# Kernel tuning notes

Measured on AMD Instinct MI355X. Metric: run time of the kernel, lower is better.

The kernel has to match this reference:

```python
import jax, jax.numpy as jnp
import numpy as np

N, E = 50000, 800000
IN_DIM, HID, HEADS, LAYERS = 128, 128, 4, 2
C = HID // HEADS  # per-head channels
LN_EPS = 1e-5


def _segment_softmax(logits, seg, num_segments):
    # logits: [E, H], seg: [E] target-node ids
    m = jax.ops.segment_max(logits, seg, num_segments=num_segments)  # [N, H]
    ex = jnp.exp(logits - m[seg])
    s = jax.ops.segment_sum(ex, seg, num_segments=num_segments)      # [N, H]
    return ex / s[seg]


def setup_inputs() -> dict:
    key = jax.random.key(0)
    ks = jax.random.split(key, 16)
    x = jax.random.normal(ks[0], (N, IN_DIM), dtype=jnp.float32)
    edge_index = jax.random.randint(ks[1], (2, E), 0, N, dtype=jnp.int64)
    edge_weight = jax.random.normal(ks[2], (E,), dtype=jnp.float32)
    s = 0.05
    # stacked per-layer params (in_ch == hidden for both layers since in_dim == hidden_dim)
    Wq = jax.random.normal(ks[3], (LAYERS, HID, HID), dtype=jnp.float32) * s
    bq = jnp.zeros((LAYERS, HID), dtype=jnp.float32)
    Wk = jax.random.normal(ks[4], (LAYERS, HID, HID), dtype=jnp.float32) * s
    bk = jnp.zeros((LAYERS, HID), dtype=jnp.float32)
    Wv = jax.random.normal(ks[5], (LAYERS, HID, HID), dtype=jnp.float32) * s
    bv = jnp.zeros((LAYERS, HID), dtype=jnp.float32)
    We = jax.random.normal(ks[6], (LAYERS, 1, HID), dtype=jnp.float32) * s  # lin_edge, no bias
    Wskip = jax.random.normal(ks[7], (LAYERS, HID, HID), dtype=jnp.float32) * s
    bskip = jnp.zeros((LAYERS, HID), dtype=jnp.float32)
    ln_g = jnp.ones((LAYERS, HID), dtype=jnp.float32)
    ln_b = jnp.zeros((LAYERS, HID), dtype=jnp.float32)
    return dict(x=x, edge_index=edge_index, edge_weight=edge_weight,
                Wq=Wq, bq=bq, Wk=Wk, bk=bk, Wv=Wv, bv=bv, We=We,
                Wskip=Wskip, bskip=bskip, ln_g=ln_g, ln_b=ln_b)


def reference(x, edge_index, edge_weight, Wq, bq, Wk, bk, Wv, bv, We, Wskip, bskip, ln_g, ln_b):
    # eval mode: dropout (on alpha and on features) is identity
    h = jnp.nan_to_num(x, nan=0.0, posinf=0.0, neginf=0.0)
    edge_attr = jnp.nan_to_num(edge_weight, nan=0.0, posinf=0.0, neginf=0.0)[:, None]  # [E,1]
    src, dst = edge_index[0], edge_index[1]  # PyG: x_j = x[src], softmax/aggregate over dst
    scale = 1.0 / jnp.sqrt(jnp.asarray(C, dtype=h.dtype))
    for l in range(LAYERS):
        h_res = h
        q = (h @ Wq[l] + bq[l]).reshape(N, HEADS, C)
        k = (h @ Wk[l] + bk[l]).reshape(N, HEADS, C)
        v = (h @ Wv[l] + bv[l]).reshape(N, HEADS, C)
        e = (edge_attr @ We[l]).reshape(E, HEADS, C)          # lin_edge (bias=False)
        kj = k[src] + e                                       # [E,H,C]
        logits = jnp.einsum('ehc,ehc->eh', q[dst], kj) * scale
        alpha = _segment_softmax(logits, dst, N)              # [E,H]
        msg = (v[src] + e) * alpha[..., None]                 # [E,H,C]
        out = jax.ops.segment_sum(msg, dst, num_segments=N).reshape(N, HID)
        out = out + h @ Wskip[l] + bskip[l]                   # root_weight skip (beta=False)
        out = jnp.nan_to_num(out, nan=0.0, posinf=0.0, neginf=0.0)
        mu = out.mean(axis=-1, keepdims=True)
        var = ((out - mu) ** 2).mean(axis=-1, keepdims=True)
        out = (out - mu) / jnp.sqrt(var + LN_EPS) * ln_g[l] + ln_b[l]
        out = jax.nn.relu(jnp.nan_to_num(out, nan=0.0, posinf=0.0, neginf=0.0))
        out = jnp.nan_to_num(out, nan=0.0, posinf=0.0, neginf=0.0)
        h = jnp.nan_to_num(out + h_res, nan=0.0, posinf=0.0, neginf=0.0)
    return h
```

## Files before the change

kernel.cpp:

```cpp
#include <hip/hip_runtime.h>
#include <hip/hip_fp16.h>
#include <math.h>

#define NN 50000
#define EE 800000
#define HID 128
#define LAYERS 2
#define LN_EPS 1e-5f
#define SCALE 0.17677669529663687f
#define NB 49

typedef _Float16 f16x8 __attribute__((ext_vector_type(8)));
typedef _Float16 h2 __attribute__((ext_vector_type(2)));
typedef float f32x4 __attribute__((ext_vector_type(4)));

__device__ __forceinline__ float sanitize(float f) {
    return (f == f && fabsf(f) != INFINITY) ? f : 0.0f;
}


__global__ void zero_deg_kernel(int* __restrict__ deg) {
    int i = blockIdx.x * blockDim.x + threadIdx.x;
    if (i < NN) deg[i] = 0;
}

__global__ void hist_kernel(const int* __restrict__ eidx, int* __restrict__ deg) {
    int e = blockIdx.x * blockDim.x + threadIdx.x;
    if (e < EE) atomicAdd(&deg[eidx[EE + e]], 1);
}


__global__ __launch_bounds__(1024) void deg_bsum_kernel(const int* __restrict__ deg,
                                                        int* __restrict__ bsum) {
    __shared__ int red[16];
    int tid = threadIdx.x;
    int i = blockIdx.x * 1024 + tid;
    int v = (i < NN) ? deg[i] : 0;
    #pragma unroll
    for (int off = 32; off >= 1; off >>= 1) v += __shfl_xor(v, off, 64);
    if ((tid & 63) == 0) red[tid >> 6] = v;
    __syncthreads();
    if (tid == 0) {
        int s = 0;
        #pragma unroll
        for (int w = 0; w < 16; ++w) s += red[w];
        bsum[blockIdx.x] = s;
    }
}

__global__ void bsum_scan_kernel(const int* __restrict__ bsum, int* __restrict__ boff,
                                 int* __restrict__ row_start) {
    int lane = threadIdx.x;
    int v = (lane < NB) ? bsum[lane] : 0;
    int sc = v;
    #pragma unroll
    for (int off = 1; off < 64; off <<= 1) {
        int t = __shfl_up(sc, off, 64);
        if (lane >= off) sc += t;
    }
    if (lane < NB) boff[lane] = sc - v;
    if (lane == 63) row_start[NN] = sc;
}

__global__ __launch_bounds__(1024) void deg_scan_kernel(const int* __restrict__ deg,
                                                        const int* __restrict__ boff,
                                                        int* __restrict__ row_start,
                                                        int* __restrict__ cursor) {
    __shared__ int wsum[16];
    int tid = threadIdx.x;
    int lane = tid & 63;
    int wid = tid >> 6;
    int i = blockIdx.x * 1024 + tid;
    int val = (i < NN) ? deg[i] : 0;
    int sc = val;
    #pragma unroll
    for (int off = 1; off < 64; off <<= 1) {
        int t = __shfl_up(sc, off, 64);
        if (lane >= off) sc += t;
    }
    if (lane == 63) wsum[wid] = sc;
    __syncthreads();
    if (wid == 0) {
        int s = (lane < 16) ? wsum[lane] : 0;
        #pragma unroll
        for (int off = 1; off < 16; off <<= 1) {
            int t = __shfl_up(s, off, 64);
            if (lane >= off) s += t;
        }
        if (lane < 16) wsum[lane] = s;
    }
    __syncthreads();
    int waveoff = (wid > 0) ? wsum[wid - 1] : 0;
    int excl = boff[blockIdx.x] + waveoff + sc - val;
    if (i < NN) {
        row_start[i] = excl;
        cursor[i] = excl;
    }
}

__global__ void scatter_kernel(const int* __restrict__ eidx,
                               const float* __restrict__ ew,
                               int* __restrict__ cursor,
                               long long* __restrict__ csr_pk) {
    int e = blockIdx.x * blockDim.x + threadIdx.x;
    if (e < EE) {
        int dst = eidx[EE + e];
        int src = eidx[e];
        int pos = atomicAdd(&cursor[dst], 1);
        unsigned wb = __float_as_uint(sanitize(ew[e]));
        csr_pk[pos] = ((long long)wb << 32) | (unsigned)src;
    }
}


__global__ void sanitize_kernel(const float* __restrict__ x, float* __restrict__ h0,
                                __half* __restrict__ hh) {
    int i = blockIdx.x * blockDim.x + threadIdx.x;
    if (i < NN * HID / 4) {
        float4 f = ((const float4*)x)[i];
        f.x = sanitize(f.x); f.y = sanitize(f.y); f.z = sanitize(f.z); f.w = sanitize(f.w);
        ((float4*)h0)[i] = f;
        __half2* hp = (__half2*)(hh + (size_t)i * 4);
        hp[0] = __floats2half2_rn(f.x, f.y);
        hp[1] = __floats2half2_rn(f.z, f.w);
    }
}


__global__ void wtcvt_kernel(const float* __restrict__ Wq, const float* __restrict__ Wk,
                             const float* __restrict__ Wv, const float* __restrict__ Wsk,
                             __half* __restrict__ WT) {
    int idx = blockIdx.x * blockDim.x + threadIdx.x;
    if (idx >= LAYERS * 4 * HID * HID) return;
    int k = idx & 127;
    int c = (idx >> 7) & 127;
    int m = (idx >> 14) & 3;
    int l = idx >> 16;
    const float* W = (m == 0) ? Wq : (m == 1) ? Wk : (m == 2) ? Wv : Wsk;
    WT[idx] = __float2half(W[l * HID * HID + k * HID + c]);
}


__global__ __launch_bounds__(256) void mfma_qkvs_kernel(
    const __half* __restrict__ hh, const __half* __restrict__ WT,
    const float* __restrict__ bq, const float* __restrict__ bk,
    const float* __restrict__ bv, const float* __restrict__ bsk,
    __half* __restrict__ qh, __half* __restrict__ kv, float* __restrict__ skf)
{
    int wid = threadIdx.x >> 6;
    int lane = threadIdx.x & 63;
    int row0 = blockIdx.x * 64 + wid * 16;
    int arow = row0 + (lane & 15);
    if (arow >= NN) arow = NN - 1;
    int ksub = (lane >> 4) * 8;

    const _Float16* hp = (const _Float16*)(hh + (size_t)arow * HID + ksub);
    f16x8 a0 = *(const f16x8*)(hp + 0);
    f16x8 a1 = *(const f16x8*)(hp + 32);
    f16x8 a2 = *(const f16x8*)(hp + 64);
    f16x8 a3 = *(const f16x8*)(hp + 96);

    #pragma unroll
    for (int m = 0; m < 4; ++m) {
        const _Float16* Wm = (const _Float16*)(WT + m * HID * HID);
        const float* bias = (m == 0) ? bq : (m == 1) ? bk : (m == 2) ? bv : bsk;
        #pragma unroll
        for (int t = 0; t < 8; ++t) {
            int col = t * 16 + (lane & 15);
            const _Float16* wc = Wm + (size_t)col * HID + ksub;
            f32x4 acc = {0.f, 0.f, 0.f, 0.f};
            acc = __builtin_amdgcn_mfma_f32_16x16x32_f16(a0, *(const f16x8*)(wc + 0),  acc, 0, 0, 0);
            acc = __builtin_amdgcn_mfma_f32_16x16x32_f16(a1, *(const f16x8*)(wc + 32), acc, 0, 0, 0);
            acc = __builtin_amdgcn_mfma_f32_16x16x32_f16(a2, *(const f16x8*)(wc + 64), acc, 0, 0, 0);
            acc = __builtin_amdgcn_mfma_f32_16x16x32_f16(a3, *(const f16x8*)(wc + 96), acc, 0, 0, 0);
            float bcol = bias[col];
            #pragma unroll
            for (int r = 0; r < 4; ++r) {
                int row = row0 + (lane >> 4) * 4 + r;
                if (row < NN) {
                    float val = acc[r] + bcol;
                    if (m == 0)      qh[(size_t)row * HID + col] = __float2half(val);
                    else if (m == 1) kv[(size_t)row * 256 + col] = __float2half(val);
                    else if (m == 2) kv[(size_t)row * 256 + 128 + col] = __float2half(val);
                    else             skf[(size_t)row * HID + col] = val;
                }
            }
        }
    }
}


struct OS8 { float m, s, tw; float a[8]; };

__device__ __forceinline__ void os8_init(OS8& o) {
    o.m = -INFINITY; o.s = 0.f; o.tw = 0.f;
    #pragma unroll
    for (int j = 0; j < 8; ++j) o.a[j] = 0.f;
}

__device__ __forceinline__ OS8 os8_mrg(OS8 a, OS8 b) {
    float mn = fmaxf(a.m, b.m);
    if (mn == -INFINITY) return a;
    float ca = __expf(a.m - mn);
    float cb = __expf(b.m - mn);
    OS8 r;
    r.m = mn;
    r.s  = a.s  * ca + b.s  * cb;
    r.tw = a.tw * ca + b.tw * cb;
    #pragma unroll
    for (int j = 0; j < 8; ++j) r.a[j] = a.a[j] * ca + b.a[j] * cb;
    return r;
}

__device__ __forceinline__ OS8 os8_shfl_xor(const OS8& o, int mask) {
    OS8 r;
    r.m  = __shfl_xor(o.m,  mask, 64);
    r.s  = __shfl_xor(o.s,  mask, 64);
    r.tw = __shfl_xor(o.tw, mask, 64);
    #pragma unroll
    for (int j = 0; j < 8; ++j) r.a[j] = __shfl_xor(o.a[j], mask, 64);
    return r;
}

__device__ __forceinline__ void edge_step(long long p, const __half* __restrict__ kv, int c0,
                                          h2 q01, h2 q23, h2 q45, h2 q67, float qwe, OS8& st) {
    int src = (int)(p & 0xffffffffLL);
    float w = __uint_as_float((unsigned)((unsigned long long)p >> 32));
    const _Float16* kvp = (const _Float16*)(kv + (size_t)src * 256);
    f16x8 k8 = *(const f16x8*)(kvp + c0);
    f16x8 v8 = *(const f16x8*)(kvp + 128 + c0);
    h2 k01 = {k8[0], k8[1]}, k23 = {k8[2], k8[3]}, k45 = {k8[4], k8[5]}, k67 = {k8[6], k8[7]};
    float d = __builtin_amdgcn_fdot2(k01, q01, 0.f, false);
    d = __builtin_amdgcn_fdot2(k23, q23, d, false);
    d = __builtin_amdgcn_fdot2(k45, q45, d, false);
    d = __builtin_amdgcn_fdot2(k67, q67, d, false);
    d += __shfl_xor(d, 1, 64);
    d += __shfl_xor(d, 2, 64);
    float l = fmaf(w, qwe, d) * SCALE;
    float mn = fmaxf(st.m, l);
    float cr = __expf(st.m - mn);
    float pp = __expf(l - mn);
    st.s  = fmaf(st.s,  cr, pp);
    st.tw = fmaf(st.tw, cr, pp * w);
    #pragma unroll
    for (int j = 0; j < 8; ++j) st.a[j] = fmaf(st.a[j], cr, pp * (float)v8[j]);
    st.m = mn;
}

__global__ __launch_bounds__(256) void agg_kernel(
    const __half* __restrict__ qh, const __half* __restrict__ kv,
    const float* __restrict__ skp, const float* __restrict__ hres,
    const float* __restrict__ We,
    const float* __restrict__ ln_g, const float* __restrict__ ln_b,
    const int* __restrict__ row_start, const long long* __restrict__ csr_pk,
    float* __restrict__ hout, __half* __restrict__ hh_out)
{
    int node = blockIdx.x * 4 + (threadIdx.x >> 6);
    int lane = threadIdx.x & 63;
    int grp = lane >> 4;
    int sl = lane & 15;
    int c0 = sl * 8;

    f16x8 q8 = *(const f16x8*)((const _Float16*)qh + (size_t)node * HID + c0);
    h2 q01 = {q8[0], q8[1]}, q23 = {q8[2], q8[3]}, q45 = {q8[4], q8[5]}, q67 = {q8[6], q8[7]};

    float4 weA = *(const float4*)(We + c0);
    float4 weB = *(const float4*)(We + c0 + 4);
    float qwe = (float)q8[0] * weA.x + (float)q8[1] * weA.y + (float)q8[2] * weA.z + (float)q8[3] * weA.w
              + (float)q8[4] * weB.x + (float)q8[5] * weB.y + (float)q8[6] * weB.z + (float)q8[7] * weB.w;
    qwe += __shfl_xor(qwe, 1, 64);
    qwe += __shfl_xor(qwe, 2, 64);

    int rs = row_start[node];
    int re = row_start[node + 1];

    OS8 s0, s1;
    os8_init(s0); os8_init(s1);

    int i = rs + grp;
    for (; i + 4 < re; i += 8) {
        long long p0 = csr_pk[i];
        long long p1 = csr_pk[i + 4];
        edge_step(p0, kv, c0, q01, q23, q45, q67, qwe, s0);
        edge_step(p1, kv, c0, q01, q23, q45, q67, qwe, s1);
    }
    if (i < re) edge_step(csr_pk[i], kv, c0, q01, q23, q45, q67, qwe, s0);

    OS8 st = os8_mrg(s0, s1);
    st = os8_mrg(st, os8_shfl_xor(st, 16));
    st = os8_mrg(st, os8_shfl_xor(st, 32));

    float inv = (re > rs) ? 1.f / st.s : 0.f;
    float wef[8] = {weA.x, weA.y, weA.z, weA.w, weB.x, weB.y, weB.z, weB.w};

    float4 skA = *(const float4*)(skp + (size_t)node * HID + c0);
    float4 skB = *(const float4*)(skp + (size_t)node * HID + c0 + 4);
    float skv[8] = {skA.x, skA.y, skA.z, skA.w, skB.x, skB.y, skB.z, skB.w};

    float ox[8];
    float sum8 = 0.f;
    #pragma unroll
    for (int j = 0; j < 8; ++j) {
        float o = fmaf(st.tw, wef[j], st.a[j]) * inv;
        o = sanitize(o + skv[j]);
        ox[j] = o;
        sum8 += o;
    }

    float mu = sum8;
    mu += __shfl_xor(mu, 1, 64); mu += __shfl_xor(mu, 2, 64);
    mu += __shfl_xor(mu, 4, 64); mu += __shfl_xor(mu, 8, 64);
    mu *= (1.f / 128.f);

    float var8 = 0.f;
    #pragma unroll
    for (int j = 0; j < 8; ++j) {
        float dx = ox[j] - mu;
        var8 = fmaf(dx, dx, var8);
    }
    float var = var8;
    var += __shfl_xor(var, 1, 64); var += __shfl_xor(var, 2, 64);
    var += __shfl_xor(var, 4, 64); var += __shfl_xor(var, 8, 64);
    var *= (1.f / 128.f);
    float rstd = rsqrtf(var + LN_EPS);

    if (grp == 0) {
        float4 gA = *(const float4*)(ln_g + c0);
        float4 gB = *(const float4*)(ln_g + c0 + 4);
        float4 bA = *(const float4*)(ln_b + c0);
        float4 bB = *(const float4*)(ln_b + c0 + 4);
        float gv[8] = {gA.x, gA.y, gA.z, gA.w, gB.x, gB.y, gB.z, gB.w};
        float bv_[8] = {bA.x, bA.y, bA.z, bA.w, bB.x, bB.y, bB.z, bB.w};

        float4 hrA = *(const float4*)(hres + (size_t)node * HID + c0);
        float4 hrB = *(const float4*)(hres + (size_t)node * HID + c0 + 4);
        float hr[8] = {hrA.x, hrA.y, hrA.z, hrA.w, hrB.x, hrB.y, hrB.z, hrB.w};

        float outv[8];
        _Float16 outh[8];
        #pragma unroll
        for (int j = 0; j < 8; ++j) {
            float rx = fmaxf(fmaf((ox[j] - mu) * rstd, gv[j], bv_[j]), 0.f);
            float o = sanitize(rx + hr[j]);
            outv[j] = o;
            outh[j] = (_Float16)o;
        }
        float* op = hout + (size_t)node * HID + c0;
        *(float4*)(op)     = make_float4(outv[0], outv[1], outv[2], outv[3]);
        *(float4*)(op + 4) = make_float4(outv[4], outv[5], outv[6], outv[7]);
        *(f16x8*)((_Float16*)hh_out + (size_t)node * HID + c0) = *(f16x8*)outh;
    }
}


extern "C" void kernel_launch(void* const* d_in, const int* in_sizes, int n_in,
                              void* d_out, int out_size, void* d_ws, size_t ws_size,
                              hipStream_t stream) {
    const float* x      = (const float*)d_in[0];
    const int*   ei     = (const int*)d_in[1];
    const float* ew     = (const float*)d_in[2];
    const float* Wq     = (const float*)d_in[3];
    const float* bq     = (const float*)d_in[4];
    const float* Wk     = (const float*)d_in[5];
    const float* bk     = (const float*)d_in[6];
    const float* Wv     = (const float*)d_in[7];
    const float* bv     = (const float*)d_in[8];
    const float* We     = (const float*)d_in[9];
    const float* Wsk    = (const float*)d_in[10];
    const float* bsk    = (const float*)d_in[11];
    const float* ln_g   = (const float*)d_in[12];
    const float* ln_b   = (const float*)d_in[13];

    const size_t NH = (size_t)NN * HID;
    float* h0  = (float*)d_ws;
    float* h1  = h0 + NH;
    float* skf = h1 + NH;
    __half* hh = (__half*)(skf + NH);
    __half* qh = hh + NH;
    __half* kv = qh + NH;
    __half* WT = kv + 2 * NH;
    int* deg       = (int*)(WT + LAYERS * 4 * HID * HID);
    int* row_start = deg + NN;
    int* cursor    = row_start + NN + 2;
    int* bsum      = cursor + NN;
    int* boff      = bsum + 64;
    long long* csr_pk = (long long*)(boff + 64);

    zero_deg_kernel<<<(NN + 255) / 256, 256, 0, stream>>>(deg);
    hist_kernel<<<(EE + 255) / 256, 256, 0, stream>>>(ei, deg);
    deg_bsum_kernel<<<NB, 1024, 0, stream>>>(deg, bsum);
    bsum_scan_kernel<<<1, 64, 0, stream>>>(bsum, boff, row_start);
    deg_scan_kernel<<<NB, 1024, 0, stream>>>(deg, boff, row_start, cursor);
    scatter_kernel<<<(EE + 255) / 256, 256, 0, stream>>>(ei, ew, cursor, csr_pk);

    sanitize_kernel<<<(NN * HID / 4 + 255) / 256, 256, 0, stream>>>(x, h0, hh);
    wtcvt_kernel<<<(LAYERS * 4 * HID * HID + 255) / 256, 256, 0, stream>>>(Wq, Wk, Wv, Wsk, WT);

    const int WELEM = HID * HID;
    const int MROWS = (NN + 63) / 64;

    for (int l = 0; l < LAYERS; ++l) {
        const float* hin = (l == 0) ? h0 : h1;
        float* hout = (l == 0) ? h1 : (float*)d_out;
        mfma_qkvs_kernel<<<MROWS, 256, 0, stream>>>(
            hh, WT + (size_t)l * 4 * WELEM,
            bq + l * HID, bk + l * HID, bv + l * HID, bsk + l * HID,
            qh, kv, skf);
        agg_kernel<<<NN / 4, 256, 0, stream>>>(
            qh, kv, skf, hin,
            We + l * HID, ln_g + l * HID, ln_b + l * HID,
            row_start, csr_pk, hout, hh);
    }
}
```

Baseline: 469.7 us.

## Stage GEMM outputs through LDS for vectorized stores and store skip in fp16

The QKV/skip GEMM kernel now writes each wave's 16x128 output tile to shared memory and then emits coalesced 16-byte vector stores, replacing scattered 2- and 4-byte per-element stores. The skip projection is also stored as fp16 instead of fp32, which halves its write and read traffic in the GEMM and aggregation kernels. This lowers the skip term's precision, and the last row tile now stores all 16 rows without a per-row bound check, which may write past NN if NN is not a multiple of 16. No barrier is used since each wave reads back only its own staging region.

```diff
diff --git a/kernel.cpp b/kernel.cpp
--- a/kernel.cpp
+++ b/kernel.cpp
@@ -145,8 +145,10 @@
     const __half* __restrict__ hh, const __half* __restrict__ WT,
     const float* __restrict__ bq, const float* __restrict__ bk,
     const float* __restrict__ bv, const float* __restrict__ bsk,
-    __half* __restrict__ qh, __half* __restrict__ kv, float* __restrict__ skf)
+    __half* __restrict__ qh, __half* __restrict__ kv, __half* __restrict__ skf)
 {
+    __shared__ _Float16 stg[4][16][HID];
+
     int wid = threadIdx.x >> 6;
     int lane = threadIdx.x & 63;
     int row0 = blockIdx.x * 64 + wid * 16;
@@ -176,13 +178,26 @@
             float bcol = bias[col];
             #pragma unroll
             for (int r = 0; r < 4; ++r) {
-                int row = row0 + (lane >> 4) * 4 + r;
-                if (row < NN) {
-                    float val = acc[r] + bcol;
-                    if (m == 0)      qh[(size_t)row * HID + col] = __float2half(val);
-                    else if (m == 1) kv[(size_t)row * 256 + col] = __float2half(val);
-                    else if (m == 2) kv[(size_t)row * 256 + 128 + col] = __float2half(val);
-                    else             skf[(size_t)row * HID + col] = val;
+                stg[wid][(lane >> 4) * 4 + r][col] = (_Float16)(acc[r] + bcol);
+            }
+        }
+        if (row0 < NN) {
+            const _Float16* s = &stg[wid][0][0];
+            if (m == 0 || m == 3) {
+                _Float16* dst = (_Float16*)(m == 0 ? qh : skf) + (size_t)row0 * HID;
+                #pragma unroll
+                for (int p = 0; p < 4; ++p) {
+                    int idx = p * 64 + lane;
+                    *(f16x8*)(dst + idx * 8) = *(const f16x8*)(s + idx * 8);
+                }
+            } else {
+                _Float16* base = (_Float16*)kv + (size_t)row0 * 256 + (m == 1 ? 0 : 128);
+                #pragma unroll
+                for (int p = 0; p < 4; ++p) {
+                    int idx = p * 64 + lane;
+                    int r = idx >> 4;
+                    int c8 = (idx & 15) * 8;
+                    *(f16x8*)(base + (size_t)r * 256 + c8) = *(const f16x8*)(s + r * HID + c8);
                 }
             }
         }
@@ -249,7 +264,7 @@
 
 __global__ __launch_bounds__(256) void agg_kernel(
     const __half* __restrict__ qh, const __half* __restrict__ kv,
-    const float* __restrict__ skp, const float* __restrict__ hres,
+    const __half* __restrict__ skp, const float* __restrict__ hres,
     const float* __restrict__ We,
     const float* __restrict__ ln_g, const float* __restrict__ ln_b,
     const int* __restrict__ row_start, const long long* __restrict__ csr_pk,
@@ -293,16 +308,14 @@
     float inv = (re > rs) ? 1.f / st.s : 0.f;
     float wef[8] = {weA.x, weA.y, weA.z, weA.w, weB.x, weB.y, weB.z, weB.w};
 
-    float4 skA = *(const float4*)(skp + (size_t)node * HID + c0);
-    float4 skB = *(const float4*)(skp + (size_t)node * HID + c0 + 4);
-    float skv[8] = {skA.x, skA.y, skA.z, skA.w, skB.x, skB.y, skB.z, skB.w};
+    f16x8 sk8 = *(const f16x8*)((const _Float16*)skp + (size_t)node * HID + c0);
 
     float ox[8];
     float sum8 = 0.f;
     #pragma unroll
     for (int j = 0; j < 8; ++j) {
         float o = fmaf(st.tw, wef[j], st.a[j]) * inv;
-        o = sanitize(o + skv[j]);
+        o = sanitize(o + (float)sk8[j]);
         ox[j] = o;
         sum8 += o;
     }
@@ -374,8 +387,8 @@
     const size_t NH = (size_t)NN * HID;
     float* h0  = (float*)d_ws;
     float* h1  = h0 + NH;
-    float* skf = h1 + NH;
-    __half* hh = (__half*)(skf + NH);
+    __half* skf = (__half*)(h1 + NH);
+    __half* hh = skf + NH;
     __half* qh = hh + NH;
     __half* kv = qh + NH;
     __half* WT = kv + 2 * NH;
```

After: 459.9 us. 1.02x faster.
